# Optimization experiments

Hardware: AMD Instinct MI355X
Metric: run time of the kernel (lower is better)

## Reference

```python
import jax, jax.numpy as jnp
import numpy as np

EMBED_DIM = 1024
N_HEADS = 16
DK = EMBED_DIM // N_HEADS


def setup_inputs() -> dict:
    key = jax.random.key(0)
    ks = jax.random.split(key, 9)
    s = 1.0 / np.sqrt(EMBED_DIM)
    d = EMBED_DIM
    return {
        "x": jax.random.normal(ks[0], (2, 2048, d), dtype=jnp.float32),
        "Wq": jax.random.uniform(ks[1], (d, d), jnp.float32, -s, s),
        "bq": jax.random.uniform(ks[2], (d,), jnp.float32, -s, s),
        "Wk": jax.random.uniform(ks[3], (d, d), jnp.float32, -s, s),
        "bk": jax.random.uniform(ks[4], (d,), jnp.float32, -s, s),
        "Wv": jax.random.uniform(ks[5], (d, d), jnp.float32, -s, s),
        "bv": jax.random.uniform(ks[6], (d,), jnp.float32, -s, s),
        "Wo": jax.random.uniform(ks[7], (d, d), jnp.float32, -s, s),
        "bo": jax.random.uniform(ks[8], (d,), jnp.float32, -s, s),
    }


def reference(x, Wq, bq, Wk, bk, Wv, bv, Wo, bo):
    B, S, D = x.shape
    H, dk = N_HEADS, DK
    # QKV projections
    q = (x @ Wq + bq).reshape(B, S, H, dk).transpose(0, 2, 1, 3)  # [B,H,S,dk]
    k = (x @ Wk + bk).reshape(B, S, H, dk).transpose(0, 2, 1, 3)
    v = (x @ Wv + bv).reshape(B, S, H, dk).transpose(0, 2, 1, 3)
    # scaled dot-product attention with full score matrix (faithful to source)
    scores = jnp.einsum("bhqd,bhkd->bhqk", q, k) / jnp.sqrt(jnp.float32(dk))
    attn = jax.nn.softmax(scores, axis=-1)
    out = jnp.einsum("bhqk,bhkd->bhqd", attn, v)  # [B,H,S,dk]
    out = out.transpose(0, 2, 1, 3).reshape(B, S, D)
    return out @ Wo + bo
```

## Files before the change

kernel.cpp:

```cpp
#include <hip/hip_runtime.h>

typedef unsigned short u16;
typedef unsigned int u32;
typedef __attribute__((ext_vector_type(8))) short short8;
typedef __attribute__((ext_vector_type(4))) float float4v;

struct alignas(8) U16x4 { u16 x, y, z, w; };

__device__ __forceinline__ u16 f2b(float f) {
    union { float f; unsigned int u; } v; v.f = f;
    unsigned int r = (v.u >> 16) & 1u;
    v.u += 0x7fffu + r;
    return (u16)(v.u >> 16);
}

__device__ __forceinline__ void gld16(const u16* g, u16* l) {
    __builtin_amdgcn_global_load_lds(
        (const __attribute__((address_space(1))) void*)g,
        (__attribute__((address_space(3))) void*)l, 16, 0, 0);
}

__device__ __forceinline__ short8 frag8(const u16* base, int row, int cg) {
    return *(const short8*)(base + row * 64 + ((cg ^ (row & 7)) << 3));
}

__global__ __launch_bounds__(256) void cvt_kernel(const float* __restrict__ in,
                                                  u16* __restrict__ out) {
    size_t i = ((size_t)blockIdx.x * 256 + threadIdx.x) * 4;
    float4 v = *(const float4*)(in + i);
    U16x4 o;
    o.x = f2b(v.x); o.y = f2b(v.y); o.z = f2b(v.z); o.w = f2b(v.w);
    *(U16x4*)(out + i) = o;
}

__global__ __launch_bounds__(256) void transpose_cvt4_kernel(
    const float* __restrict__ W0, const float* __restrict__ W1,
    const float* __restrict__ W2, const float* __restrict__ W3,
    u16* __restrict__ T0, u16* __restrict__ T1,
    u16* __restrict__ T2, u16* __restrict__ T3) {
    __shared__ float tile[32][33];
    int z = blockIdx.z;
    const float* W = (z == 0) ? W0 : (z == 1) ? W1 : (z == 2) ? W2 : W3;
    u16* T = (z == 0) ? T0 : (z == 1) ? T1 : (z == 2) ? T2 : T3;
    int t = threadIdx.x;
    int tx = t & 31, ty = t >> 5;
    int bk = blockIdx.y * 32, bn = blockIdx.x * 32;
#pragma unroll
    for (int p = 0; p < 4; ++p) {
        int k = ty + p * 8;
        tile[k][tx] = W[(size_t)(bk + k) * 1024 + bn + tx];
    }
    __syncthreads();
#pragma unroll
    for (int p = 0; p < 4; ++p) {
        int n = ty + p * 8;
        T[(size_t)(bn + n) * 1024 + bk + tx] = f2b(tile[tx][n]);
    }
}

__device__ __forceinline__ void gemm_core_gld(const u16* __restrict__ A,
                                              const u16* __restrict__ BT,
                                              int m0, int n0, int t,
                                              u16* As, u16* Bs,
                                              float4v acc[4][4]) {
    int lane = t & 63, wid = t >> 6;
    int wr = wid >> 1, wc = wid & 1;
    int l16 = lane & 15, quad = lane >> 4;
    int rl = lane >> 3, cs = lane & 7;

    for (int k0 = 0; k0 < 1024; k0 += 64) {
        __syncthreads();
#pragma unroll
        for (int p = 0; p < 4; ++p) {
            int blk = wid * 4 + p;
            int row = blk * 8 + rl;
            int c = cs ^ (row & 7);
            gld16(A + (size_t)(m0 + row) * 1024 + k0 + c * 8, As + blk * 512);
            gld16(BT + (size_t)(n0 + row) * 1024 + k0 + c * 8, Bs + blk * 512);
        }
        __syncthreads();
#pragma unroll
        for (int ks = 0; ks < 64; ks += 32) {
            int cg = (ks >> 3) + quad;
            short8 af[4], bf[4];
#pragma unroll
            for (int i = 0; i < 4; ++i) af[i] = frag8(As, wr * 64 + i * 16 + l16, cg);
#pragma unroll
            for (int j = 0; j < 4; ++j) bf[j] = frag8(Bs, wc * 64 + j * 16 + l16, cg);
#pragma unroll
            for (int i = 0; i < 4; ++i)
#pragma unroll
                for (int j = 0; j < 4; ++j)
                    acc[i][j] = __builtin_amdgcn_mfma_f32_16x16x32_bf16(
                        af[i], bf[j], acc[i][j], 0, 0, 0);
        }
    }
}

__global__ __launch_bounds__(256) void qkv_kernel(
    const u16* __restrict__ X,
    const u16* __restrict__ WqT, const u16* __restrict__ WkT, const u16* __restrict__ WvT,
    const float* __restrict__ bq, const float* __restrict__ bk, const float* __restrict__ bv,
    u16* __restrict__ Qo, u16* __restrict__ Ko, u16* __restrict__ VTo) {
    __shared__ __align__(16) u16 As[128 * 64];
    __shared__ __align__(16) u16 Bs[128 * 64];
    int id = blockIdx.x;
    int m = (id & 7) | (((id >> 3) & 3) << 3);
    int nz = id >> 5;
    int n = nz & 7, z = nz >> 3;
    const u16* BT = (z == 0) ? WqT : (z == 1) ? WkT : WvT;
    const float* bias = (z == 0) ? bq : (z == 1) ? bk : bv;
    int t = threadIdx.x;
    int m0 = m * 128, n0 = n * 128;

    float4v acc[4][4];
    float4v zero4 = {0.f, 0.f, 0.f, 0.f};
#pragma unroll
    for (int i = 0; i < 4; ++i)
#pragma unroll
        for (int j = 0; j < 4; ++j) acc[i][j] = zero4;

    gemm_core_gld(X, BT, m0, n0, t, As, Bs, acc);

    int lane = t & 63, wid = t >> 6;
    int wr = wid >> 1, wc = wid & 1;
    int l16 = lane & 15, quad = lane >> 4;
    float scale = (z == 0) ? 0.18033688011112042f : 1.0f;

#pragma unroll
    for (int j = 0; j < 4; ++j) {
        int n1 = n0 + wc * 64 + j * 16 + l16;
        float bvl = bias[n1];
#pragma unroll
        for (int i = 0; i < 4; ++i) {
            int mbase = m0 + wr * 64 + i * 16 + quad * 4;
            if (z < 2) {
                u16* out = (z == 0) ? Qo : Ko;
#pragma unroll
                for (int r = 0; r < 4; ++r)
                    out[(size_t)(mbase + r) * 1024 + n1] =
                        f2b((acc[i][j][r] + bvl) * scale);
            } else {
                int bidx = mbase >> 11, s = mbase & 2047;
                size_t base =
                    ((size_t)((bidx * 16 + (n1 >> 6)) * 64 + (n1 & 63))) * 2048 + s;
                U16x4 pk;
                pk.x = f2b(acc[i][j][0] + bvl);
                pk.y = f2b(acc[i][j][1] + bvl);
                pk.z = f2b(acc[i][j][2] + bvl);
                pk.w = f2b(acc[i][j][3] + bvl);
                *(U16x4*)(VTo + base) = pk;
            }
        }
    }
}

__global__ __launch_bounds__(256) void oproj_kernel(const u16* __restrict__ X,
                                                    const u16* __restrict__ WoT,
                                                    const float* __restrict__ bias,
                                                    float* __restrict__ out) {
    __shared__ __align__(16) u16 As[128 * 64];
    __shared__ __align__(16) u16 Bs[128 * 64];
    int id = blockIdx.x;
    int m = (id & 7) | (((id >> 3) & 3) << 3);
    int n = id >> 5;
    int t = threadIdx.x;
    int m0 = m * 128, n0 = n * 128;

    float4v acc[4][4];
    float4v zero4 = {0.f, 0.f, 0.f, 0.f};
#pragma unroll
    for (int i = 0; i < 4; ++i)
#pragma unroll
        for (int j = 0; j < 4; ++j) acc[i][j] = zero4;

    gemm_core_gld(X, WoT, m0, n0, t, As, Bs, acc);

    int lane = t & 63, wid = t >> 6;
    int wr = wid >> 1, wc = wid & 1;
    int l16 = lane & 15, quad = lane >> 4;

#pragma unroll
    for (int j = 0; j < 4; ++j) {
        int n1 = n0 + wc * 64 + j * 16 + l16;
        float bvl = bias[n1];
#pragma unroll
        for (int i = 0; i < 4; ++i) {
            int mbase = m0 + wr * 64 + i * 16 + quad * 4;
#pragma unroll
            for (int r = 0; r < 4; ++r)
                out[(size_t)(mbase + r) * 1024 + n1] = acc[i][j][r] + bvl;
        }
    }
}

__global__ __launch_bounds__(128) void flash_kernel(const u16* __restrict__ Q,
                                                    const u16* __restrict__ Kn,
                                                    const u16* __restrict__ VT,
                                                    float* __restrict__ Opart,
                                                    float* __restrict__ lpart) {
    __shared__ __align__(16) u16 Ks[64 * 64];
    __shared__ __align__(16) u16 Vs[64 * 64];
    __shared__ __align__(16) u16 Ps[64][72];

    int id = blockIdx.x;
    int bh = (id & 7) | (((id >> 3) & 3) << 3);
    int rest = id >> 5;
    int qb = rest & 31, kvz = rest >> 5;
    int b = bh >> 4, h = bh & 15;
    int t = threadIdx.x;
    int wid = t >> 6, lane = t & 63;
    int l16 = lane & 15, quad = lane >> 4;
    int rl = lane >> 3, cs = lane & 7;
    int q0 = qb * 64 + wid * 32;
    size_t kbase = (size_t)(b * 2048) * 1024 + h * 64;
    size_t vbase = (size_t)(bh * 64) * 2048;

    short8 qf[2][2];
#pragma unroll
    for (int j = 0; j < 2; ++j)
#pragma unroll
        for (int kk = 0; kk < 2; ++kk)
            qf[j][kk] = *(const short8*)(
                Q + ((size_t)(b * 2048 + q0 + j * 16 + l16)) * 1024 + h * 64 +
                kk * 32 + quad * 8);

    float4v oacc[2][4], lacc[2];
    float4v zero4 = {0.f, 0.f, 0.f, 0.f};
#pragma unroll
    for (int ip = 0; ip < 2; ++ip) {
        lacc[ip] = zero4;
#pragma unroll
        for (int jd = 0; jd < 4; ++jd) oacc[ip][jd] = zero4;
    }

    const short ONE = (short)0x3F80;
    short8 ones = {ONE, ONE, ONE, ONE, ONE, ONE, ONE, ONE};

    for (int kvi = 0; kvi < 16; ++kvi) {
        int kv = kvz * 1024 + kvi * 64;
        __syncthreads();
        if (wid == 0) {
#pragma unroll
            for (int p = 0; p < 8; ++p) {
                int row = p * 8 + rl;
                int c = cs ^ (row & 7);
                gld16(Kn + kbase + (size_t)(kv + row) * 1024 + c * 8, Ks + p * 512);
            }
        } else {
#pragma unroll
            for (int p = 0; p < 8; ++p) {
                int row = p * 8 + rl;
                int c = cs ^ (row & 7);
                gld16(VT + vbase + (size_t)row * 2048 + kv + c * 8, Vs + p * 512);
            }
        }
        __syncthreads();

        float4v sacc[4][2];
#pragma unroll
        for (int i = 0; i < 4; ++i)
#pragma unroll
            for (int j = 0; j < 2; ++j) sacc[i][j] = zero4;
#pragma unroll
        for (int kk = 0; kk < 2; ++kk) {
            int cg = kk * 4 + quad;
            short8 kf[4];
#pragma unroll
            for (int i = 0; i < 4; ++i) kf[i] = frag8(Ks, i * 16 + l16, cg);
#pragma unroll
            for (int i = 0; i < 4; ++i)
#pragma unroll
                for (int j = 0; j < 2; ++j)
                    sacc[i][j] = __builtin_amdgcn_mfma_f32_16x16x32_bf16(
                        kf[i], qf[j][kk], sacc[i][j], 0, 0, 0);
        }

#pragma unroll
        for (int i = 0; i < 4; ++i)
#pragma unroll
            for (int j = 0; j < 2; ++j) {
                u32 e0 = __float_as_uint(__builtin_amdgcn_exp2f(sacc[i][j][0])) + 0x8000u;
                u32 e1 = __float_as_uint(__builtin_amdgcn_exp2f(sacc[i][j][1])) + 0x8000u;
                u32 e2 = __float_as_uint(__builtin_amdgcn_exp2f(sacc[i][j][2])) + 0x8000u;
                u32 e3 = __float_as_uint(__builtin_amdgcn_exp2f(sacc[i][j][3])) + 0x8000u;
                uint2 pk;
                pk.x = __builtin_amdgcn_perm(e1, e0, 0x07060302u);
                pk.y = __builtin_amdgcn_perm(e3, e2, 0x07060302u);
                *(uint2*)(&Ps[wid * 32 + j * 16 + l16][i * 16 + quad * 4]) = pk;
            }

#pragma unroll
        for (int kk = 0; kk < 2; ++kk) {
            int cg = kk * 4 + quad;
            short8 pf[2];
#pragma unroll
            for (int ip = 0; ip < 2; ++ip)
                pf[ip] = *(const short8*)(
                    &Ps[wid * 32 + ip * 16 + l16][kk * 32 + quad * 8]);
#pragma unroll
            for (int jd = 0; jd < 4; ++jd) {
                short8 vf = frag8(Vs, jd * 16 + l16, cg);
#pragma unroll
                for (int ip = 0; ip < 2; ++ip)
                    oacc[ip][jd] = __builtin_amdgcn_mfma_f32_16x16x32_bf16(
                        pf[ip], vf, oacc[ip][jd], 0, 0, 0);
            }
#pragma unroll
            for (int ip = 0; ip < 2; ++ip)
                lacc[ip] = __builtin_amdgcn_mfma_f32_16x16x32_bf16(
                    pf[ip], ones, lacc[ip], 0, 0, 0);
        }
    }

    size_t obase = (size_t)kvz * 4194304;
#pragma unroll
    for (int ip = 0; ip < 2; ++ip)
#pragma unroll
        for (int r = 0; r < 4; ++r) {
            int q = q0 + ip * 16 + quad * 4 + r;
#pragma unroll
            for (int jd = 0; jd < 4; ++jd)
                Opart[obase + ((size_t)(b * 2048 + q)) * 1024 + h * 64 +
                      jd * 16 + l16] = oacc[ip][jd][r];
        }
    if (l16 == 0) {
#pragma unroll
        for (int ip = 0; ip < 2; ++ip)
#pragma unroll
            for (int r = 0; r < 4; ++r) {
                int q = q0 + ip * 16 + quad * 4 + r;
                lpart[kvz * 65536 + (b * 2048 + q) * 16 + h] = lacc[ip][r];
            }
    }
}

__global__ __launch_bounds__(256) void combine_kernel(const float* __restrict__ Op,
                                                      const float* __restrict__ lp,
                                                      u16* __restrict__ out) {
    int idx = blockIdx.x * 256 + threadIdx.x;
    size_t i = (size_t)idx * 4;
    int qg = idx >> 8;
    int d = (idx & 255) * 4;
    int h = d >> 6;
    float l0 = lp[qg * 16 + h], l1 = lp[65536 + qg * 16 + h];
    float inv = 1.0f / (l0 + l1);
    float4 o0 = *(const float4*)(Op + i);
    float4 o1 = *(const float4*)(Op + 4194304 + i);
    U16x4 o;
    o.x = f2b((o0.x + o1.x) * inv);
    o.y = f2b((o0.y + o1.y) * inv);
    o.z = f2b((o0.z + o1.z) * inv);
    o.w = f2b((o0.w + o1.w) * inv);
    *(U16x4*)(out + i) = o;
}

extern "C" void kernel_launch(void* const* d_in, const int* in_sizes, int n_in,
                              void* d_out, int out_size, void* d_ws, size_t ws_size,
                              hipStream_t stream) {
    const float* x  = (const float*)d_in[0];
    const float* Wq = (const float*)d_in[1];
    const float* bq = (const float*)d_in[2];
    const float* Wk = (const float*)d_in[3];
    const float* bk = (const float*)d_in[4];
    const float* Wv = (const float*)d_in[5];
    const float* bv = (const float*)d_in[6];
    const float* Wo = (const float*)d_in[7];
    const float* bo = (const float*)d_in[8];
    float* out = (float*)d_out;

    char* ws = (char*)d_ws;
    const size_t MB = 1024 * 1024;
    u16* xb  = (u16*)(ws);
    u16* wqt = (u16*)(ws + 8 * MB);
    u16* wkt = (u16*)(ws + 10 * MB);
    u16* wvt = (u16*)(ws + 12 * MB);
    u16* wot = (u16*)(ws + 14 * MB);
    u16* qb_ = (u16*)(ws + 16 * MB);
    u16* kb_ = (u16*)(ws + 24 * MB);
    u16* vt_ = (u16*)(ws + 32 * MB);
    u16* ab_ = (u16*)(ws + 40 * MB);
    float* op_ = (float*)(ws + 48 * MB);
    float* lp_ = (float*)(ws + 80 * MB);

    cvt_kernel<<<4096, 256, 0, stream>>>(x, xb);
    transpose_cvt4_kernel<<<dim3(32, 32, 4), 256, 0, stream>>>(
        Wq, Wk, Wv, Wo, wqt, wkt, wvt, wot);

    qkv_kernel<<<768, 256, 0, stream>>>(xb, wqt, wkt, wvt, bq, bk, bv,
                                        qb_, kb_, vt_);
    flash_kernel<<<2048, 128, 0, stream>>>(qb_, kb_, vt_, op_, lp_);
    combine_kernel<<<4096, 256, 0, stream>>>(op_, lp_, ab_);
    oproj_kernel<<<256, 256, 0, stream>>>(ab_, wot, bo, out);
}
```

Before: 218.8 us.

## Merge prep kernels, load V fragments directly, store bf16 partial outputs

Folds the x conversion and the weight transpose-convert into one prep kernel launch. In the flash kernel, both waves now share the K tile load into LDS, and the V^T fragments are read straight from global memory into registers instead of staged through LDS. The split-KV partial outputs are stored as bf16 rather than fp32, which halves the partial-output traffic written by flash and read by combine. This costs some precision in the partial sums and adds register pressure plus uncoalesced-ish global loads for V.

```diff
diff --git a/kernel.cpp b/kernel.cpp
--- a/kernel.cpp
+++ b/kernel.cpp
@@ -14,6 +14,10 @@
     return (u16)(v.u >> 16);
 }
 
+__device__ __forceinline__ float b2f(u16 u) {
+    union { unsigned int u; float f; } v; v.u = ((u32)u) << 16; return v.f;
+}
+
 __device__ __forceinline__ void gld16(const u16* g, u16* l) {
     __builtin_amdgcn_global_load_lds(
         (const __attribute__((address_space(1))) void*)g,
@@ -24,27 +28,29 @@
     return *(const short8*)(base + row * 64 + ((cg ^ (row & 7)) << 3));
 }
 
-__global__ __launch_bounds__(256) void cvt_kernel(const float* __restrict__ in,
-                                                  u16* __restrict__ out) {
-    size_t i = ((size_t)blockIdx.x * 256 + threadIdx.x) * 4;
-    float4 v = *(const float4*)(in + i);
-    U16x4 o;
-    o.x = f2b(v.x); o.y = f2b(v.y); o.z = f2b(v.z); o.w = f2b(v.w);
-    *(U16x4*)(out + i) = o;
-}
-
-__global__ __launch_bounds__(256) void transpose_cvt4_kernel(
-    const float* __restrict__ W0, const float* __restrict__ W1,
-    const float* __restrict__ W2, const float* __restrict__ W3,
+__global__ __launch_bounds__(256) void prep_kernel(
+    const float* __restrict__ x, const float* __restrict__ W0,
+    const float* __restrict__ W1, const float* __restrict__ W2,
+    const float* __restrict__ W3, u16* __restrict__ xb,
     u16* __restrict__ T0, u16* __restrict__ T1,
     u16* __restrict__ T2, u16* __restrict__ T3) {
     __shared__ float tile[32][33];
-    int z = blockIdx.z;
+    int id = blockIdx.x;
+    if (id < 4096) {
+        size_t i = ((size_t)id * 256 + threadIdx.x) * 4;
+        float4 v = *(const float4*)(x + i);
+        U16x4 o;
+        o.x = f2b(v.x); o.y = f2b(v.y); o.z = f2b(v.z); o.w = f2b(v.w);
+        *(U16x4*)(xb + i) = o;
+        return;
+    }
+    int r = id - 4096;
+    int z = r >> 10, tl = r & 1023;
     const float* W = (z == 0) ? W0 : (z == 1) ? W1 : (z == 2) ? W2 : W3;
     u16* T = (z == 0) ? T0 : (z == 1) ? T1 : (z == 2) ? T2 : T3;
     int t = threadIdx.x;
     int tx = t & 31, ty = t >> 5;
-    int bk = blockIdx.y * 32, bn = blockIdx.x * 32;
+    int bn = (tl & 31) * 32, bk = (tl >> 5) * 32;
 #pragma unroll
     for (int p = 0; p < 4; ++p) {
         int k = ty + p * 8;
@@ -197,10 +203,9 @@
 __global__ __launch_bounds__(128) void flash_kernel(const u16* __restrict__ Q,
                                                     const u16* __restrict__ Kn,
                                                     const u16* __restrict__ VT,
-                                                    float* __restrict__ Opart,
+                                                    u16* __restrict__ Opart,
                                                     float* __restrict__ lpart) {
     __shared__ __align__(16) u16 Ks[64 * 64];
-    __shared__ __align__(16) u16 Vs[64 * 64];
     __shared__ __align__(16) u16 Ps[64][72];
 
     int id = blockIdx.x;
@@ -240,21 +245,21 @@
     for (int kvi = 0; kvi < 16; ++kvi) {
         int kv = kvz * 1024 + kvi * 64;
         __syncthreads();
-        if (wid == 0) {
-#pragma unroll
-            for (int p = 0; p < 8; ++p) {
-                int row = p * 8 + rl;
-                int c = cs ^ (row & 7);
-                gld16(Kn + kbase + (size_t)(kv + row) * 1024 + c * 8, Ks + p * 512);
-            }
-        } else {
-#pragma unroll
-            for (int p = 0; p < 8; ++p) {
-                int row = p * 8 + rl;
-                int c = cs ^ (row & 7);
-                gld16(VT + vbase + (size_t)row * 2048 + kv + c * 8, Vs + p * 512);
-            }
-        }
+#pragma unroll
+        for (int p = 0; p < 4; ++p) {
+            int blk = wid * 4 + p;
+            int row = blk * 8 + rl;
+            int c = cs ^ (row & 7);
+            gld16(Kn + kbase + (size_t)(kv + row) * 1024 + c * 8, Ks + blk * 512);
+        }
+        short8 vf[2][4];
+#pragma unroll
+        for (int kk = 0; kk < 2; ++kk)
+#pragma unroll
+            for (int jd = 0; jd < 4; ++jd)
+                vf[kk][jd] = *(const short8*)(
+                    VT + vbase + (size_t)(jd * 16 + l16) * 2048 + kv +
+                    kk * 32 + quad * 8);
         __syncthreads();
 
         float4v sacc[4][2];
@@ -292,20 +297,17 @@
 
 #pragma unroll
         for (int kk = 0; kk < 2; ++kk) {
-            int cg = kk * 4 + quad;
             short8 pf[2];
 #pragma unroll
             for (int ip = 0; ip < 2; ++ip)
                 pf[ip] = *(const short8*)(
                     &Ps[wid * 32 + ip * 16 + l16][kk * 32 + quad * 8]);
 #pragma unroll
-            for (int jd = 0; jd < 4; ++jd) {
-                short8 vf = frag8(Vs, jd * 16 + l16, cg);
+            for (int jd = 0; jd < 4; ++jd)
 #pragma unroll
                 for (int ip = 0; ip < 2; ++ip)
                     oacc[ip][jd] = __builtin_amdgcn_mfma_f32_16x16x32_bf16(
-                        pf[ip], vf, oacc[ip][jd], 0, 0, 0);
-            }
+                        pf[ip], vf[kk][jd], oacc[ip][jd], 0, 0, 0);
 #pragma unroll
             for (int ip = 0; ip < 2; ++ip)
                 lacc[ip] = __builtin_amdgcn_mfma_f32_16x16x32_bf16(
@@ -322,7 +324,7 @@
 #pragma unroll
             for (int jd = 0; jd < 4; ++jd)
                 Opart[obase + ((size_t)(b * 2048 + q)) * 1024 + h * 64 +
-                      jd * 16 + l16] = oacc[ip][jd][r];
+                      jd * 16 + l16] = f2b(oacc[ip][jd][r]);
         }
     if (l16 == 0) {
 #pragma unroll
@@ -335,7 +337,7 @@
     }
 }
 
-__global__ __launch_bounds__(256) void combine_kernel(const float* __restrict__ Op,
+__global__ __launch_bounds__(256) void combine_kernel(const u16* __restrict__ Op,
                                                       const float* __restrict__ lp,
                                                       u16* __restrict__ out) {
     int idx = blockIdx.x * 256 + threadIdx.x;
@@ -345,13 +347,13 @@
     int h = d >> 6;
     float l0 = lp[qg * 16 + h], l1 = lp[65536 + qg * 16 + h];
     float inv = 1.0f / (l0 + l1);
-    float4 o0 = *(const float4*)(Op + i);
-    float4 o1 = *(const float4*)(Op + 4194304 + i);
+    U16x4 o0 = *(const U16x4*)(Op + i);
+    U16x4 o1 = *(const U16x4*)(Op + 4194304 + i);
     U16x4 o;
-    o.x = f2b((o0.x + o1.x) * inv);
-    o.y = f2b((o0.y + o1.y) * inv);
-    o.z = f2b((o0.z + o1.z) * inv);
-    o.w = f2b((o0.w + o1.w) * inv);
+    o.x = f2b((b2f(o0.x) + b2f(o1.x)) * inv);
+    o.y = f2b((b2f(o0.y) + b2f(o1.y)) * inv);
+    o.z = f2b((b2f(o0.z) + b2f(o1.z)) * inv);
+    o.w = f2b((b2f(o0.w) + b2f(o1.w)) * inv);
     *(U16x4*)(out + i) = o;
 }
 
@@ -380,13 +382,11 @@
     u16* kb_ = (u16*)(ws + 24 * MB);
     u16* vt_ = (u16*)(ws + 32 * MB);
     u16* ab_ = (u16*)(ws + 40 * MB);
-    float* op_ = (float*)(ws + 48 * MB);
-    float* lp_ = (float*)(ws + 80 * MB);
-
-    cvt_kernel<<<4096, 256, 0, stream>>>(x, xb);
-    transpose_cvt4_kernel<<<dim3(32, 32, 4), 256, 0, stream>>>(
-        Wq, Wk, Wv, Wo, wqt, wkt, wvt, wot);
-
+    u16* op_ = (u16*)(ws + 48 * MB);
+    float* lp_ = (float*)(ws + 64 * MB);
+
+    prep_kernel<<<8192, 256, 0, stream>>>(x, Wq, Wk, Wv, Wo, xb,
+                                          wqt, wkt, wvt, wot);
     qkv_kernel<<<768, 256, 0, stream>>>(xb, wqt, wkt, wvt, bq, bk, bv,
                                         qb_, kb_, vt_);
     flash_kernel<<<2048, 128, 0, stream>>>(qb_, kb_, vt_, op_, lp_);
```

Result: slower. 253.5 us (+15.8%).
